# Optimization experiments

Measured on AMD Instinct MI355X. Metric: run time of the kernel, lower is better.

Reference implementation:

```python
import jax, jax.numpy as jnp
import numpy as np

B, T, D, U = 64, 512, 256, 512


def setup_inputs() -> dict:
    key = jax.random.key(0)
    ks = jax.random.split(key, 7)
    s = 0.05  # keras 'uniform' init is small; small scale keeps gates unsaturated
    return {
        "x": jax.random.normal(ks[0], (B, T, D), dtype=jnp.float32),
        "w_xi": jax.random.normal(ks[1], (D, U), dtype=jnp.float32) * s,
        "w_xf": jax.random.normal(ks[2], (D, U), dtype=jnp.float32) * s,
        "w_xc": jax.random.normal(ks[3], (D, U), dtype=jnp.float32) * s,
        "w_hi": jax.random.normal(ks[4], (U, U), dtype=jnp.float32) * s,
        "w_hf": jax.random.normal(ks[5], (U, U), dtype=jnp.float32) * s,
        "w_hc": jax.random.normal(ks[6], (U, U), dtype=jnp.float32) * s,
        "b_i": jnp.zeros((1, U), dtype=jnp.float32),
        "b_f": jnp.zeros((1, U), dtype=jnp.float32),
        "b_c": jnp.zeros((1, U), dtype=jnp.float32),
        "h0": jnp.zeros((B, U), dtype=jnp.float32),
        "c0": jnp.zeros((B, U), dtype=jnp.float32),
    }


def reference(x, w_xi, w_xf, w_xc, w_hi, w_hf, w_hc, b_i, b_f, b_c, h0, c0):
    # Precompute input projections for all timesteps (batched GEMM), time-major.
    xi = (jnp.einsum('btd,du->btu', x, w_xi) + b_i).transpose(1, 0, 2)  # [T,B,U]
    xf = (jnp.einsum('btd,du->btu', x, w_xf) + b_f).transpose(1, 0, 2)
    xc = (jnp.einsum('btd,du->btu', x, w_xc) + b_c).transpose(1, 0, 2)

    def step(carry, xs):
        h, c = carry
        xi_t, xf_t, xc_t = xs
        i = jax.nn.sigmoid(xi_t + h @ w_hi)
        f = jax.nn.sigmoid(xf_t + h @ w_hf)
        c_in = jnp.tanh(xc_t + h @ w_hc)
        c_n = f * c + i * c_in
        h_n = jnp.tanh(c_n)  # output gate o == 1.0 in NOGLSTM
        return (h_n, c_n), h_n

    (_, _), hs = jax.lax.scan(step, (h0, c0), (xi, xf, xc))
    return hs.transpose(1, 0, 2)  # [B,T,U] full hidden sequence
```

## Files before the change

kernel.cpp:

```cpp
#include <hip/hip_runtime.h>
#include <stdint.h>

#define Bv 64
#define Tv 512
#define Dv 256
#define Uv 512
#define WPG 32
#define FPAD 16

typedef __attribute__((ext_vector_type(8))) __bf16 bf16x8;
typedef __attribute__((ext_vector_type(8))) short short8;
typedef __attribute__((ext_vector_type(4))) float f32x4;
typedef unsigned long long u64;

__device__ unsigned int g_flag[4 * WPG * FPAD];
__device__ unsigned int g_gen[4 * WPG];
__device__ u64 g_hbuf[2 * Bv * Uv / 2];

__device__ __forceinline__ unsigned int f2bf_bits(float x) {
    unsigned int u = __float_as_uint(x);
    return (u + 0x7fffu + ((u >> 16) & 1u)) >> 16;
}
__device__ __forceinline__ float bfbits2f(unsigned int b) {
    return __uint_as_float(b << 16);
}
__device__ __forceinline__ float fast_sigmoid(float x) {
    return __builtin_amdgcn_rcpf(1.f + __expf(-x));
}
__device__ __forceinline__ float fast_tanh(float x) {
    float ax = fabsf(x);
    float t  = __expf(-2.f * ax);
    float r  = (1.f - t) * __builtin_amdgcn_rcpf(1.f + t);
    return x < 0.f ? -r : r;
}

extern "C" __global__ void __launch_bounds__(256, 1)
noglstm_kernel(const float* __restrict__ x,
               const float* __restrict__ w_xi, const float* __restrict__ w_xf, const float* __restrict__ w_xc,
               const float* __restrict__ w_hi, const float* __restrict__ w_hf, const float* __restrict__ w_hc,
               const float* __restrict__ b_i, const float* __restrict__ b_f, const float* __restrict__ b_c,
               const float* __restrict__ h0, const float* __restrict__ c0,
               float* __restrict__ out)
{
    __shared__ f32x4 partLds[12 * 64];
    __shared__ float cTile[256];
    __shared__ float biasLds[48];
    __shared__ unsigned int baseLds;

    const int tid  = threadIdx.x;
    const int wg   = blockIdx.x;
    const int g    = wg >> 5;
    const int c    = wg & 31;
    const int r0   = g * 16;
    const int u0   = c * 16;
    const int wv   = tid >> 6;
    const int lane = tid & 63;
    const int n    = lane & 15;
    const int quad = lane >> 4;
    const int kh   = wv;
    const int m    = n;
    const int q    = quad;

    if (tid == 0) { unsigned v = g_gen[wg] + 1u; g_gen[wg] = v; baseLds = (v - 1u) * (unsigned)Tv; }
    if (tid < 16)      biasLds[tid]      = b_i[u0 + tid];
    else if (tid < 32) biasLds[tid]      = b_f[u0 + tid - 16];
    else if (tid < 48) biasLds[tid]      = b_c[u0 + tid - 32];
    cTile[tid] = c0[(size_t)(r0 + (tid >> 4)) * Uv + u0 + (tid & 15)];

    const float* WhP[3] = {w_hi, w_hf, w_hc};
    const float* WxP[3] = {w_xi, w_xf, w_xc};
    const int ucol = u0 + n;

    bf16x8 whHiR[3][4], whLoR[3][4], wxHiR[3][2], wxLoR[3][2];
    #pragma unroll
    for (int nt = 0; nt < 3; ++nt) {
        #pragma unroll
        for (int i = 0; i < 4; ++i) {
            short8 hi8, lo8;
            #pragma unroll
            for (int e = 0; e < 8; ++e) {
                int k = (kh * 4 + i) * 32 + quad * 8 + e;
                float w = WhP[nt][(size_t)k * Uv + ucol];
                unsigned int hb = f2bf_bits(w);
                unsigned int lb = f2bf_bits(w - bfbits2f(hb));
                hi8[e] = (short)hb; lo8[e] = (short)lb;
            }
            whHiR[nt][i] = __builtin_bit_cast(bf16x8, hi8);
            whLoR[nt][i] = __builtin_bit_cast(bf16x8, lo8);
        }
        #pragma unroll
        for (int i = 0; i < 2; ++i) {
            short8 hi8, lo8;
            #pragma unroll
            for (int e = 0; e < 8; ++e) {
                int k = (kh * 2 + i) * 32 + quad * 8 + e;
                float w = WxP[nt][(size_t)k * Uv + ucol];
                unsigned int hb = f2bf_bits(w);
                unsigned int lb = f2bf_bits(w - bfbits2f(hb));
                hi8[e] = (short)hb; lo8[e] = (short)lb;
            }
            wxHiR[nt][i] = __builtin_bit_cast(bf16x8, hi8);
            wxLoR[nt][i] = __builtin_bit_cast(bf16x8, lo8);
        }
    }

    f32x4 xf[4];
    #pragma unroll
    for (int i = 0; i < 2; ++i) {
        int kt = kh * 2 + i;
        const float* p = x + ((size_t)(r0 + m) * Tv + 0) * Dv + kt * 32 + q * 8;
        xf[i * 2]     = *(const f32x4*)p;
        xf[i * 2 + 1] = *(const f32x4*)(p + 4);
    }
    __syncthreads();
    const unsigned int base = baseLds;

    const unsigned int* fpw = g_flag + (size_t)(g * WPG + kh * 8) * FPAD;

    for (int t = 0; t < Tv; ++t) {
        const bool packed = (t != 0);
        const bool pfch = (t + 1 < Tv);
        u64 hw64[16];
        f32x4 hf[8];

        if (packed) {
            const unsigned int E = base + (unsigned)t;
            unsigned int fv = 0xFFFFFFFFu;
            unsigned int spins = 0;
            for (;;) {
                if (lane < 8)
                    fv = __hip_atomic_load(fpw + (size_t)lane * FPAD,
                                           __ATOMIC_RELAXED, __HIP_MEMORY_SCOPE_AGENT);
                if (__all((lane >= 8) || (fv >= E))) break;
                if (++spins > (1u << 20)) break;
                if (spins > 16) __builtin_amdgcn_s_sleep(1);
            }
            __asm__ volatile("" ::: "memory");

            const u64* hb = g_hbuf + (size_t)((t - 1) & 1) * (Bv * Uv / 2);
            #pragma unroll
            for (int i = 0; i < 4; ++i) {
                int kt = kh * 4 + i;
                const u64* p = hb + (size_t)(kt * 16 + q * 4) * Bv + r0 + m;
                #pragma unroll
                for (int j = 0; j < 4; ++j)
                    hw64[i * 4 + j] = __hip_atomic_load(p + (size_t)j * Bv,
                                                        __ATOMIC_RELAXED,
                                                        __HIP_MEMORY_SCOPE_AGENT);
            }
        } else {
            #pragma unroll
            for (int i = 0; i < 4; ++i) {
                int kt = kh * 4 + i;
                const float* p = h0 + (size_t)(r0 + m) * Uv + kt * 32 + q * 8;
                hf[i * 2]     = *(const f32x4*)p;
                hf[i * 2 + 1] = *(const f32x4*)(p + 4);
            }
        }

        bf16x8 xaH[2], xaL[2];
        #pragma unroll
        for (int i = 0; i < 2; ++i) {
            short8 hi8, lo8;
            #pragma unroll
            for (int e = 0; e < 8; ++e) {
                float v = (e < 4) ? xf[i * 2][e] : xf[i * 2 + 1][e - 4];
                unsigned int hb2 = f2bf_bits(v);
                unsigned int lb2 = f2bf_bits(v - bfbits2f(hb2));
                hi8[e] = (short)hb2; lo8[e] = (short)lb2;
            }
            xaH[i] = __builtin_bit_cast(bf16x8, hi8);
            xaL[i] = __builtin_bit_cast(bf16x8, lo8);
        }

        f32x4 acc[3], accX[3];
        #pragma unroll
        for (int nt = 0; nt < 3; ++nt) { acc[nt] = f32x4{0.f,0.f,0.f,0.f}; accX[nt] = f32x4{0.f,0.f,0.f,0.f}; }
        #pragma unroll
        for (int i = 0; i < 2; ++i) {
            #pragma unroll
            for (int nt = 0; nt < 3; ++nt) {
                accX[nt] = __builtin_amdgcn_mfma_f32_16x16x32_bf16(xaH[i], wxHiR[nt][i], accX[nt], 0, 0, 0);
                accX[nt] = __builtin_amdgcn_mfma_f32_16x16x32_bf16(xaH[i], wxLoR[nt][i], accX[nt], 0, 0, 0);
                accX[nt] = __builtin_amdgcn_mfma_f32_16x16x32_bf16(xaL[i], wxHiR[nt][i], accX[nt], 0, 0, 0);
                accX[nt] = __builtin_amdgcn_mfma_f32_16x16x32_bf16(xaL[i], wxLoR[nt][i], accX[nt], 0, 0, 0);
            }
        }

        #pragma unroll
        for (int i = 0; i < 4; ++i) {
            bf16x8 haH, haL;
            if (packed) {
                short8 hi8, lo8;
                #pragma unroll
                for (int j = 0; j < 4; ++j) {
                    u64 w = hw64[i * 4 + j];
                    unsigned int d0 = (unsigned int)w;
                    unsigned int d1 = (unsigned int)(w >> 32);
                    hi8[2 * j]     = (short)(d0 >> 16);
                    lo8[2 * j]     = (short)(d0 & 0xffffu);
                    hi8[2 * j + 1] = (short)(d1 >> 16);
                    lo8[2 * j + 1] = (short)(d1 & 0xffffu);
                }
                haH = __builtin_bit_cast(bf16x8, hi8);
                haL = __builtin_bit_cast(bf16x8, lo8);
            } else {
                short8 hi8, lo8;
                #pragma unroll
                for (int e = 0; e < 8; ++e) {
                    float v = (e < 4) ? hf[i * 2][e] : hf[i * 2 + 1][e - 4];
                    unsigned int hb2 = f2bf_bits(v);
                    unsigned int lb2 = f2bf_bits(v - bfbits2f(hb2));
                    hi8[e] = (short)hb2; lo8[e] = (short)lb2;
                }
                haH = __builtin_bit_cast(bf16x8, hi8);
                haL = __builtin_bit_cast(bf16x8, lo8);
            }
            #pragma unroll
            for (int nt = 0; nt < 3; ++nt) {
                acc[nt] = __builtin_amdgcn_mfma_f32_16x16x32_bf16(haH, whHiR[nt][i], acc[nt], 0, 0, 0);
                acc[nt] = __builtin_amdgcn_mfma_f32_16x16x32_bf16(haH, whLoR[nt][i], acc[nt], 0, 0, 0);
                acc[nt] = __builtin_amdgcn_mfma_f32_16x16x32_bf16(haL, whHiR[nt][i], acc[nt], 0, 0, 0);
                acc[nt] = __builtin_amdgcn_mfma_f32_16x16x32_bf16(haL, whLoR[nt][i], acc[nt], 0, 0, 0);
            }
        }

        #pragma unroll
        for (int nt = 0; nt < 3; ++nt) {
            acc[nt][0] += accX[nt][0]; acc[nt][1] += accX[nt][1];
            acc[nt][2] += accX[nt][2]; acc[nt][3] += accX[nt][3];
            partLds[(wv * 3 + nt) * 64 + lane] = acc[nt];
        }
        __syncthreads();

        const int r = tid >> 4, uu = tid & 15;
        float hn;
        {
            int plane = (r >> 2) * 16 + uu;
            int reg = r & 3;
            const float* pf2 = (const float*)partLds;
            float pi = biasLds[uu], pF = biasLds[16 + uu], pc = biasLds[32 + uu];
            #pragma unroll
            for (int w = 0; w < 4; ++w) {
                pi += pf2[((w * 3 + 0) * 64 + plane) * 4 + reg];
                pF += pf2[((w * 3 + 1) * 64 + plane) * 4 + reg];
                pc += pf2[((w * 3 + 2) * 64 + plane) * 4 + reg];
            }
            float iv  = fast_sigmoid(pi);
            float fv  = fast_sigmoid(pF);
            float cin = fast_tanh(pc);
            float cn  = fv * cTile[tid] + iv * cin;
            cTile[tid] = cn;
            hn = fast_tanh(cn);
            unsigned int hbb = f2bf_bits(hn);
            unsigned int lbb = f2bf_bits(hn - bfbits2f(hbb));
            unsigned int* hb32 = (unsigned int*)g_hbuf;
            size_t di = (size_t)(t & 1) * (Bv * Uv)
                      + ((size_t)((u0 + uu) >> 1) * Bv + (r0 + r)) * 2 + (uu & 1);
            __hip_atomic_store(hb32 + di, (hbb << 16) | lbb, __ATOMIC_RELAXED,
                               __HIP_MEMORY_SCOPE_AGENT);
        }

        __asm__ volatile("s_waitcnt vmcnt(0)" ::: "memory");
        __syncthreads();
        if (tid == 0)
            __hip_atomic_store(&g_flag[(size_t)(g * WPG + c) * FPAD],
                               base + (unsigned)t + 1u,
                               __ATOMIC_RELAXED, __HIP_MEMORY_SCOPE_AGENT);

        out[((size_t)(r0 + r) * Tv + t) * Uv + u0 + uu] = hn;

        if (pfch) {
            #pragma unroll
            for (int i = 0; i < 2; ++i) {
                int kt = kh * 2 + i;
                const float* p = x + ((size_t)(r0 + m) * Tv + (t + 1)) * Dv + kt * 32 + q * 8;
                xf[i * 2]     = *(const f32x4*)p;
                xf[i * 2 + 1] = *(const f32x4*)(p + 4);
            }
        }
    }
}

extern "C" void kernel_launch(void* const* d_in, const int* in_sizes, int n_in,
                              void* d_out, int out_size, void* d_ws, size_t ws_size,
                              hipStream_t stream) {
    (void)in_sizes; (void)n_in; (void)out_size; (void)d_ws; (void)ws_size;
    noglstm_kernel<<<dim3(128), dim3(256), 0, stream>>>(
        (const float*)d_in[0],
        (const float*)d_in[1], (const float*)d_in[2], (const float*)d_in[3],
        (const float*)d_in[4], (const float*)d_in[5], (const float*)d_in[6],
        (const float*)d_in[7], (const float*)d_in[8], (const float*)d_in[9],
        (const float*)d_in[10], (const float*)d_in[11],
        (float*)d_out);
}
```

Before: 1.870 ms.

## Replace end-of-step barrier with LDS counter release and double-buffer partials

Drops the second __syncthreads per timestep. Each wave now bumps an LDS counter, and the last wave to arrive publishes the global step flag. The partial-sum LDS buffer is double-buffered by step parity so the next step's writes cannot race reads from the current step. The flag poll is also issued speculatively at the end of the previous step to hide its latency. This cuts per-step barrier cost on the serial recurrence critical path, but relies on the LDS counter ordering being correct across waves.

After: 1.888 ms. No clear change (+0.9%).

```diff
diff --git a/kernel.cpp b/kernel.cpp
--- a/kernel.cpp
+++ b/kernel.cpp
@@ -42,10 +42,11 @@
                const float* __restrict__ h0, const float* __restrict__ c0,
                float* __restrict__ out)
 {
-    __shared__ f32x4 partLds[12 * 64];
+    __shared__ f32x4 partLds[2][12 * 64];
     __shared__ float cTile[256];
     __shared__ float biasLds[48];
     __shared__ unsigned int baseLds;
+    __shared__ unsigned int relCnt;
 
     const int tid  = threadIdx.x;
     const int wg   = blockIdx.x;
@@ -61,7 +62,10 @@
     const int m    = n;
     const int q    = quad;
 
-    if (tid == 0) { unsigned v = g_gen[wg] + 1u; g_gen[wg] = v; baseLds = (v - 1u) * (unsigned)Tv; }
+    if (tid == 0) {
+        unsigned v = g_gen[wg] + 1u; g_gen[wg] = v; baseLds = (v - 1u) * (unsigned)Tv;
+        relCnt = 0u;
+    }
     if (tid < 16)      biasLds[tid]      = b_i[u0 + tid];
     else if (tid < 32) biasLds[tid]      = b_f[u0 + tid - 16];
     else if (tid < 48) biasLds[tid]      = b_c[u0 + tid - 32];
@@ -117,23 +121,26 @@
 
     const unsigned int* fpw = g_flag + (size_t)(g * WPG + kh * 8) * FPAD;
 
+    unsigned int fvP = 0;
+
     for (int t = 0; t < Tv; ++t) {
         const bool packed = (t != 0);
         const bool pfch = (t + 1 < Tv);
+        const int par = t & 1;
         u64 hw64[16];
         f32x4 hf[8];
 
         if (packed) {
             const unsigned int E = base + (unsigned)t;
-            unsigned int fv = 0xFFFFFFFFu;
+            unsigned int fv = fvP;
             unsigned int spins = 0;
             for (;;) {
+                if (__all((lane >= 8) || (fv >= E))) break;
+                if (++spins > (1u << 20)) break;
+                if (spins > 16) __builtin_amdgcn_s_sleep(1);
                 if (lane < 8)
                     fv = __hip_atomic_load(fpw + (size_t)lane * FPAD,
                                            __ATOMIC_RELAXED, __HIP_MEMORY_SCOPE_AGENT);
-                if (__all((lane >= 8) || (fv >= E))) break;
-                if (++spins > (1u << 20)) break;
-                if (spins > 16) __builtin_amdgcn_s_sleep(1);
             }
             __asm__ volatile("" ::: "memory");
 
@@ -229,7 +236,7 @@
         for (int nt = 0; nt < 3; ++nt) {
             acc[nt][0] += accX[nt][0]; acc[nt][1] += accX[nt][1];
             acc[nt][2] += accX[nt][2]; acc[nt][3] += accX[nt][3];
-            partLds[(wv * 3 + nt) * 64 + lane] = acc[nt];
+            partLds[par][(wv * 3 + nt) * 64 + lane] = acc[nt];
         }
         __syncthreads();
 
@@ -238,7 +245,7 @@
         {
             int plane = (r >> 2) * 16 + uu;
             int reg = r & 3;
-            const float* pf2 = (const float*)partLds;
+            const float* pf2 = (const float*)partLds[par];
             float pi = biasLds[uu], pF = biasLds[16 + uu], pc = biasLds[32 + uu];
             #pragma unroll
             for (int w = 0; w < 4; ++w) {
@@ -247,26 +254,28 @@
                 pc += pf2[((w * 3 + 2) * 64 + plane) * 4 + reg];
             }
             float iv  = fast_sigmoid(pi);
-            float fv  = fast_sigmoid(pF);
+            float fv2 = fast_sigmoid(pF);
             float cin = fast_tanh(pc);
-            float cn  = fv * cTile[tid] + iv * cin;
+            float cn  = fv2 * cTile[tid] + iv * cin;
             cTile[tid] = cn;
             hn = fast_tanh(cn);
             unsigned int hbb = f2bf_bits(hn);
             unsigned int lbb = f2bf_bits(hn - bfbits2f(hbb));
             unsigned int* hb32 = (unsigned int*)g_hbuf;
-            size_t di = (size_t)(t & 1) * (Bv * Uv)
+            size_t di = (size_t)par * (Bv * Uv)
                       + ((size_t)((u0 + uu) >> 1) * Bv + (r0 + r)) * 2 + (uu & 1);
             __hip_atomic_store(hb32 + di, (hbb << 16) | lbb, __ATOMIC_RELAXED,
                                __HIP_MEMORY_SCOPE_AGENT);
         }
 
         __asm__ volatile("s_waitcnt vmcnt(0)" ::: "memory");
-        __syncthreads();
-        if (tid == 0)
-            __hip_atomic_store(&g_flag[(size_t)(g * WPG + c) * FPAD],
-                               base + (unsigned)t + 1u,
-                               __ATOMIC_RELAXED, __HIP_MEMORY_SCOPE_AGENT);
+        if (lane == 0) {
+            unsigned int old = atomicAdd(&relCnt, 1u);
+            if (old == 4u * (unsigned)(t + 1) - 1u)
+                __hip_atomic_store(&g_flag[(size_t)(g * WPG + c) * FPAD],
+                                   base + (unsigned)t + 1u,
+                                   __ATOMIC_RELAXED, __HIP_MEMORY_SCOPE_AGENT);
+        }
 
         out[((size_t)(r0 + r) * Tv + t) * Uv + u0 + uu] = hn;
 
@@ -278,6 +287,9 @@
                 xf[i * 2]     = *(const f32x4*)p;
                 xf[i * 2 + 1] = *(const f32x4*)(p + 4);
             }
+            if (lane < 8)
+                fvP = __hip_atomic_load(fpw + (size_t)lane * FPAD,
+                                        __ATOMIC_RELAXED, __HIP_MEMORY_SCOPE_AGENT);
         }
     }
 }
```
